# Performance work log

Hardware: AMD Instinct MI355X
Metric: run time of the kernel (lower is better)

The kernel has to match this reference:

```python
import jax, jax.numpy as jnp
import numpy as np

M, K, N, G = 2048, 1024, 1024, 64


def _dequant(weight, scale, offset):
    # Ascend antiquant: w_fp = (w_int + offset) * scale, per group g and out-channel n
    return (weight.astype(scale.dtype) + offset[:, None, :]) * scale[:, None, :]  # [G,K,N]


def _grouped_dot(x, w, group_sizes):
    # x:[M,K], w:[G,K,N], group_sizes:[G] (rows of x are contiguous per group)
    if hasattr(jax.lax, "ragged_dot"):
        return jax.lax.ragged_dot(x, w, group_sizes.astype(jnp.int32))
    # fallback for older jax: groups are equal-sized in this setup
    g = w.shape[0]
    m = x.shape[0] // g
    return jnp.einsum('gmk,gkn->gmn', x.reshape(g, m, -1), w).reshape(x.shape[0], -1)


def setup_inputs() -> dict:
    key = jax.random.key(0)
    k1, k2, k3, k4 = jax.random.split(key, 4)
    x = jax.random.normal(k1, (M, K), dtype=jnp.float32)
    weight = jax.random.randint(k2, (G, K, N), -8, 8, dtype=jnp.int32)
    antiquant_scale = jax.random.uniform(k3, (G, N), dtype=jnp.float32, minval=0.005, maxval=0.02)
    antiquant_offset = jax.random.normal(k4, (G, N), dtype=jnp.float32)
    # group_list_type == 0 -> cumulative row counts, last entry == M (equal groups here)
    group_list = (jnp.arange(1, G + 1, dtype=jnp.int64) * (M // G))
    return {
        "x": x,
        "weight": weight,
        "antiquant_scale": antiquant_scale,
        "antiquant_offset": antiquant_offset,
        "group_list": group_list,
        "group_list_type": 0,
    }


def reference(x, weight, antiquant_scale, antiquant_offset, group_list, group_list_type):
    w_fp = _dequant(weight, antiquant_scale, antiquant_offset)  # [G,K,N]
    if group_list_type == 0:  # cumulative -> per-group sizes
        group_sizes = jnp.diff(group_list, prepend=jnp.zeros((1,), group_list.dtype))
    else:  # already per-group counts
        group_sizes = group_list
    return _grouped_dot(x, w_fp, group_sizes)  # [M,N]
```

## Files before the change

kernel.cpp:

```cpp
#include <hip/hip_runtime.h>

constexpr int Kdim = 1024;
constexpr int Ndim = 1024;
constexpr int Gdim = 64;
constexpr int ROWS = 32;
constexpr size_t KSTEP_BYTES = 16ull * Ndim * 4;

typedef float          f32x16 __attribute__((ext_vector_type(16)));
typedef __bf16         bf16x8 __attribute__((ext_vector_type(8)));
typedef unsigned short u16x4  __attribute__((ext_vector_type(4)));
typedef unsigned short u16x8  __attribute__((ext_vector_type(8)));

static __device__ __forceinline__ unsigned short f2bf_rne(float f) {
  unsigned u = __float_as_uint(f);
  u += 0x7FFFu + ((u >> 16) & 1u);
  return (unsigned short)(u >> 16);
}

__global__ __launch_bounds__(512)
void gmm_wq_kernel(const float* __restrict__ x,
                   const int*   __restrict__ w,
                   const float* __restrict__ scale,
                   const float* __restrict__ offs,
                   const void*  __restrict__ gl_raw,
                   const int*   __restrict__ glt,
                   float*       __restrict__ out)
{
  __shared__ __align__(16) unsigned short xs[ROWS * Kdim];
  __shared__ float xsum[ROWS];

  const int tid  = threadIdx.x;
  const int b    = blockIdx.x;
  const int slot = b >> 3;
  const int g     = (b & 7) * 8 + (slot >> 2);
  const int nbase = (slot & 3) << 8;

  const int*       gl32 = (const int*)gl_raw;
  const long long* gl64 = (const long long*)gl_raw;
  const bool is64 = (gl32[1] == 0);
  auto glv = [&](int i) -> long long { return is64 ? gl64[i] : (long long)gl32[i]; };
  int row_start, rows;
  if (glt[0] == 0) {
    long long prev = (g == 0) ? 0 : glv(g - 1);
    row_start = (int)prev;
    rows      = (int)(glv(g) - prev);
  } else {
    long long s = 0;
    for (int i = 0; i < g; ++i) s += glv(i);
    row_start = (int)s;
    rows      = (int)glv(g);
  }
  rows = (rows > ROWS) ? ROWS : rows;

  const int lane  = tid & 63;
  const int wave  = tid >> 6;
  const int n0    = nbase + wave * 32;
  const int nlane = lane & 31;
  const int khalf = lane >> 5;

  const char* wbase = (const char*)w + (size_t)g * Kdim * Ndim * 4;
  int woff[8];
  #pragma unroll
  for (int e = 0; e < 8; ++e)
    woff[e] = ((khalf * 8 + e) * Ndim + n0 + nlane) * 4;

  auto loadW = [&](const char* p, int (&d)[8]) {
    #pragma unroll
    for (int e = 0; e < 8; ++e)
      d[e] = __builtin_nontemporal_load((const int*)(p + woff[e]));
  };

  int Wa[8], Wb[8], Wc[8];
  loadW(wbase,                   Wa);
  loadW(wbase +     KSTEP_BYTES, Wb);
  loadW(wbase + 2 * KSTEP_BYTES, Wc);

  {
    const int r   = tid >> 4;
    const int c16 = tid & 15;
    const bool valid = (r < rows);
    const float4* xr = (const float4*)(x + (size_t)(row_start + r) * Kdim);
    const int swz = (r & 7) << 4;
    char* base = (char*)xs + r * (Kdim * 2);
    float psum = 0.f;
    #pragma unroll
    for (int it = 0; it < 16; ++it) {
      const int c4 = c16 + it * 16;
      float4 v = make_float4(0.f, 0.f, 0.f, 0.f);
      if (valid) v = xr[c4];
      u16x4 h;
      h.x = f2bf_rne(v.x); h.y = f2bf_rne(v.y);
      h.z = f2bf_rne(v.z); h.w = f2bf_rne(v.w);
      *(u16x4*)(base + ((c4 * 8) ^ swz)) = h;
      psum += __uint_as_float((unsigned)h.x << 16)
            + __uint_as_float((unsigned)h.y << 16)
            + __uint_as_float((unsigned)h.z << 16)
            + __uint_as_float((unsigned)h.w << 16);
    }
    #pragma unroll
    for (int m = 8; m >= 1; m >>= 1) psum += __shfl_xor(psum, m);
    if (c16 == 0) xsum[r] = psum;
  }
  __syncthreads();

  const int abase = nlane * (Kdim * 2) + khalf * 16;
  const int axor  = (nlane & 7) << 4;
  const char* xsb = (const char*)xs;

  f32x16 acc;
  #pragma unroll
  for (int i = 0; i < 16; ++i) acc[i] = 0.f;

  auto cvtW = [&](const int (&s)[8]) -> bf16x8 {
    u16x8 r;
    #pragma unroll
    for (int e = 0; e < 8; ++e)
      r[e] = (unsigned short)(__float_as_uint((float)s[e]) >> 16);
    return __builtin_bit_cast(bf16x8, r);
  };
  auto ldsA = [&](int kk) -> bf16x8 {
    return *(const bf16x8*)(xsb + ((abase + kk * 32) ^ axor));
  };

  for (int kk = 0; kk < 63; kk += 3) {
    const char* pf = wbase + (size_t)(kk + 3) * KSTEP_BYTES;
    {
      bf16x8 bfr = cvtW(Wa);
      if (kk + 3 < 64) loadW(pf, Wa);
      acc = __builtin_amdgcn_mfma_f32_32x32x16_bf16(ldsA(kk), bfr, acc, 0, 0, 0);
    }
    {
      bf16x8 bfr = cvtW(Wb);
      if (kk + 4 < 64) loadW(pf + KSTEP_BYTES, Wb);
      acc = __builtin_amdgcn_mfma_f32_32x32x16_bf16(ldsA(kk + 1), bfr, acc, 0, 0, 0);
    }
    {
      bf16x8 bfr = cvtW(Wc);
      if (kk + 5 < 64) loadW(pf + 2 * KSTEP_BYTES, Wc);
      acc = __builtin_amdgcn_mfma_f32_32x32x16_bf16(ldsA(kk + 2), bfr, acc, 0, 0, 0);
    }
  }
  {
    bf16x8 bfr = cvtW(Wa);
    acc = __builtin_amdgcn_mfma_f32_32x32x16_bf16(ldsA(63), bfr, acc, 0, 0, 0);
  }

  const int col = n0 + nlane;
  const float sc = scale[g * Ndim + col];
  const float of = offs [g * Ndim + col];
  #pragma unroll
  for (int r = 0; r < 16; ++r) {
    const int rl = (r & 3) + 8 * (r >> 2) + 4 * khalf;
    if (rl < rows)
      __builtin_nontemporal_store(sc * (acc[r] + of * xsum[rl]),
                                  &out[(size_t)(row_start + rl) * Ndim + col]);
  }
}

extern "C" void kernel_launch(void* const* d_in, const int* in_sizes, int n_in,
                              void* d_out, int out_size, void* d_ws, size_t ws_size,
                              hipStream_t stream) {
  const float* x   = (const float*)d_in[0];
  const int*   w   = (const int*)d_in[1];
  const float* sc  = (const float*)d_in[2];
  const float* of  = (const float*)d_in[3];
  const void*  gl  = d_in[4];
  const int*   glt = (const int*)d_in[5];
  float*       out = (float*)d_out;

  hipLaunchKernelGGL(gmm_wq_kernel, dim3(Gdim * 4), dim3(512), 0, stream,
                     x, w, sc, of, gl, glt, out);
}
```

Baseline: 51.50 us.

## Deepen weight prefetch to eight k-steps and issue x loads before weight loads

```diff
diff --git a/kernel.cpp b/kernel.cpp
--- a/kernel.cpp
+++ b/kernel.cpp
@@ -70,27 +70,32 @@
       d[e] = __builtin_nontemporal_load((const int*)(p + woff[e]));
   };
 
-  int Wa[8], Wb[8], Wc[8];
-  loadW(wbase,                   Wa);
-  loadW(wbase +     KSTEP_BYTES, Wb);
-  loadW(wbase + 2 * KSTEP_BYTES, Wc);
+  const int r   = tid >> 4;
+  const int c16 = tid & 15;
+  const bool valid = (r < rows);
+  const float4* xr = (const float4*)(x + (size_t)(row_start + r) * Kdim);
+  float4 xv[16];
+  #pragma unroll
+  for (int it = 0; it < 16; ++it) {
+    xv[it] = make_float4(0.f, 0.f, 0.f, 0.f);
+    if (valid) xv[it] = xr[c16 + it * 16];
+  }
+
+  int W[8][8];
+  #pragma unroll
+  for (int j = 0; j < 8; ++j)
+    loadW(wbase + (size_t)j * KSTEP_BYTES, W[j]);
 
   {
-    const int r   = tid >> 4;
-    const int c16 = tid & 15;
-    const bool valid = (r < rows);
-    const float4* xr = (const float4*)(x + (size_t)(row_start + r) * Kdim);
     const int swz = (r & 7) << 4;
     char* base = (char*)xs + r * (Kdim * 2);
     float psum = 0.f;
     #pragma unroll
     for (int it = 0; it < 16; ++it) {
       const int c4 = c16 + it * 16;
-      float4 v = make_float4(0.f, 0.f, 0.f, 0.f);
-      if (valid) v = xr[c4];
       u16x4 h;
-      h.x = f2bf_rne(v.x); h.y = f2bf_rne(v.y);
-      h.z = f2bf_rne(v.z); h.w = f2bf_rne(v.w);
+      h.x = f2bf_rne(xv[it].x); h.y = f2bf_rne(xv[it].y);
+      h.z = f2bf_rne(xv[it].z); h.w = f2bf_rne(xv[it].w);
       *(u16x4*)(base + ((c4 * 8) ^ swz)) = h;
       psum += __uint_as_float((unsigned)h.x << 16)
             + __uint_as_float((unsigned)h.y << 16)
@@ -112,47 +117,34 @@
   for (int i = 0; i < 16; ++i) acc[i] = 0.f;
 
   auto cvtW = [&](const int (&s)[8]) -> bf16x8 {
-    u16x8 r;
+    u16x8 rr;
     #pragma unroll
     for (int e = 0; e < 8; ++e)
-      r[e] = (unsigned short)(__float_as_uint((float)s[e]) >> 16);
-    return __builtin_bit_cast(bf16x8, r);
+      rr[e] = (unsigned short)(__float_as_uint((float)s[e]) >> 16);
+    return __builtin_bit_cast(bf16x8, rr);
   };
   auto ldsA = [&](int kk) -> bf16x8 {
     return *(const bf16x8*)(xsb + ((abase + kk * 32) ^ axor));
   };
 
-  for (int kk = 0; kk < 63; kk += 3) {
-    const char* pf = wbase + (size_t)(kk + 3) * KSTEP_BYTES;
-    {
-      bf16x8 bfr = cvtW(Wa);
-      if (kk + 3 < 64) loadW(pf, Wa);
-      acc = __builtin_amdgcn_mfma_f32_32x32x16_bf16(ldsA(kk), bfr, acc, 0, 0, 0);
+  for (int kk = 0; kk < 64; kk += 8) {
+    #pragma unroll
+    for (int j = 0; j < 8; ++j) {
+      bf16x8 bfr = cvtW(W[j]);
+      const int next = kk + 8 + j;
+      if (next < 64) loadW(wbase + (size_t)next * KSTEP_BYTES, W[j]);
+      acc = __builtin_amdgcn_mfma_f32_32x32x16_bf16(ldsA(kk + j), bfr, acc, 0, 0, 0);
     }
-    {
-      bf16x8 bfr = cvtW(Wb);
-      if (kk + 4 < 64) loadW(pf + KSTEP_BYTES, Wb);
-      acc = __builtin_amdgcn_mfma_f32_32x32x16_bf16(ldsA(kk + 1), bfr, acc, 0, 0, 0);
-    }
-    {
-      bf16x8 bfr = cvtW(Wc);
-      if (kk + 5 < 64) loadW(pf + 2 * KSTEP_BYTES, Wc);
-      acc = __builtin_amdgcn_mfma_f32_32x32x16_bf16(ldsA(kk + 2), bfr, acc, 0, 0, 0);
-    }
-  }
-  {
-    bf16x8 bfr = cvtW(Wa);
-    acc = __builtin_amdgcn_mfma_f32_32x32x16_bf16(ldsA(63), bfr, acc, 0, 0, 0);
   }
 
   const int col = n0 + nlane;
   const float sc = scale[g * Ndim + col];
   const float of = offs [g * Ndim + col];
   #pragma unroll
-  for (int r = 0; r < 16; ++r) {
-    const int rl = (r & 3) + 8 * (r >> 2) + 4 * khalf;
+  for (int rr = 0; rr < 16; ++rr) {
+    const int rl = (rr & 3) + 8 * (rr >> 2) + 4 * khalf;
     if (rl < rows)
-      __builtin_nontemporal_store(sc * (acc[r] + of * xsum[rl]),
+      __builtin_nontemporal_store(sc * (acc[rr] + of * xsum[rl]),
                                   &out[(size_t)(row_start + rl) * Ndim + col]);
   }
 }
```

New measurement: 51.50 us. About the same (-0.0%).
